# Kernel tuning notes

Hardware: AMD Instinct MI355X
Metric: run time of the kernel (lower is better)

## Reference

```python
import jax, jax.numpy as jnp
import numpy as np


def setup_inputs() -> dict:
    key = jax.random.key(0)
    kx, kw, kb = jax.random.split(key, 3)
    x = jax.random.normal(kx, (4, 2048, 4096), dtype=jnp.float32)
    weight = jax.random.normal(kw, (4096, 4096), dtype=jnp.float32) * 0.02
    bias = jax.random.normal(kb, (4096,), dtype=jnp.float32) * 0.02
    return {"x": x, "weight": weight, "bias": bias}


def _binarize_except_outliers(w):
    # Outlier mask from global weight stats (computed from w itself; in torch it
    # is cached after the first call but the values are identical every step).
    mean = jnp.mean(w)
    std = jnp.std(w, ddof=1)  # torch.std default is the unbiased estimator
    lower = mean - 1.96 * std
    upper = mean + 1.96 * std
    outliers = (w < lower) | (w > upper)
    keep = (~outliers).astype(w.dtype)
    # scaling_factor in the torch code: w[~outliers].abs().mean(-1) on the
    # flattened masked-select -> a single SCALAR, detached from the graph.
    scale = jax.lax.stop_gradient(jnp.sum(jnp.abs(w) * keep) / jnp.sum(keep))
    # NOTE: the torch code assigns STE-sign values and then immediately
    # overwrites them with w * scale, so the effective math is:
    w_bin = jnp.where(outliers, w, w * scale)
    return w_bin


def reference(x, weight, bias):
    w_bin = _binarize_except_outliers(weight)  # [out, in]
    # F.linear(x, w, b) = x @ w.T + b
    return jnp.einsum("bsi,oi->bso", x, w_bin) + bias
```

## Files before the change

kernel.cpp:

```cpp
#include <hip/hip_runtime.h>
#include <hip/hip_bf16.h>
#include <math.h>

#define MDIM 8192
#define NDIM 4096
#define KDIM 4096
#define WELEMS 16777216
#define XELEMS 33554432

typedef __attribute__((ext_vector_type(8))) short bf16x8;
typedef __attribute__((ext_vector_type(4))) float f32x4;
typedef unsigned short ushort_t;

__device__ __forceinline__ unsigned short f2bf(float f) {
  unsigned int u = __float_as_uint(f);
  u += 0x7fffu + ((u >> 16) & 1u);
  return (unsigned short)(u >> 16);
}

__device__ __forceinline__ void gload16(const void* g, void* l) {
  __builtin_amdgcn_global_load_lds(
      (const __attribute__((address_space(1))) void*)g,
      (__attribute__((address_space(3))) void*)l, 16, 0, 0);
}

template <int MODE>
__global__ __launch_bounds__(256)
void np_stage1(const float* __restrict__ w, float* __restrict__ C,
               float* __restrict__ C2, const float* __restrict__ scal) {
  __shared__ float ls[32], ls2[32];
  const int t = threadIdx.x;
  const int leaf = t >> 3, j = t & 7;
  const size_t base = (size_t)blockIdx.x * 4096 + leaf * 128 + j;
  float mean = 0.f, lower = 0.f, upper = 0.f;
  if (MODE == 1) mean = scal[0];
  if (MODE == 2) { lower = scal[1]; upper = scal[2]; }
  float r = 0.f, r2 = 0.f;
#pragma unroll
  for (int s = 0; s < 16; s++) {
    float v = w[base + s * 8];
    float tv, tv2 = 0.f;
    if (MODE == 0) tv = v;
    else if (MODE == 1) { float x = v - mean; tv = __fmul_rn(x, x); }
    else {
      bool keep = !(v < lower || v > upper);
      tv = keep ? fabsf(v) : 0.f;
      tv2 = keep ? 1.f : 0.f;
    }
    if (s == 0) { r = tv; r2 = tv2; } else { r += tv; r2 += tv2; }
  }
  r += __shfl_xor(r, 1); r += __shfl_xor(r, 2); r += __shfl_xor(r, 4);
  if (MODE == 2) { r2 += __shfl_xor(r2, 1); r2 += __shfl_xor(r2, 2); r2 += __shfl_xor(r2, 4); }
  if (j == 0) { ls[leaf] = r; if (MODE == 2) ls2[leaf] = r2; }
  __syncthreads();
  if (t == 0) {
    float tmp[32];
    for (int i = 0; i < 32; i++) tmp[i] = ls[i];
    for (int n = 32; n > 1; n >>= 1)
      for (int i = 0; i < n / 2; i++) tmp[i] = tmp[2 * i] + tmp[2 * i + 1];
    C[blockIdx.x] = tmp[0];
    if (MODE == 2) {
      for (int i = 0; i < 32; i++) tmp[i] = ls2[i];
      for (int n = 32; n > 1; n >>= 1)
        for (int i = 0; i < n / 2; i++) tmp[i] = tmp[2 * i] + tmp[2 * i + 1];
      C2[blockIdx.x] = tmp[0];
    }
  }
}

template <int MODE>
__global__ __launch_bounds__(256)
void np_stage2(const float* __restrict__ C, const float* __restrict__ C2,
               float* __restrict__ scal) {
  __shared__ float ls[256], ls2[256];
  const int t = threadIdx.x;
  {
    float v[16];
    for (int i = 0; i < 16; i++) v[i] = C[t * 16 + i];
    for (int n = 16; n > 1; n >>= 1)
      for (int i = 0; i < n / 2; i++) v[i] = v[2 * i] + v[2 * i + 1];
    ls[t] = v[0];
    if (MODE == 2) {
      for (int i = 0; i < 16; i++) v[i] = C2[t * 16 + i];
      for (int n = 16; n > 1; n >>= 1)
        for (int i = 0; i < n / 2; i++) v[i] = v[2 * i] + v[2 * i + 1];
      ls2[t] = v[0];
    }
  }
  __syncthreads();
  if (t == 0) {
    float tmp[256];
    for (int i = 0; i < 256; i++) tmp[i] = ls[i];
    for (int n = 256; n > 1; n >>= 1)
      for (int i = 0; i < n / 2; i++) tmp[i] = tmp[2 * i] + tmp[2 * i + 1];
    float S = tmp[0];
    if (MODE == 0) {
      scal[0] = S / 16777216.0f;
    } else if (MODE == 1) {
      float var = S / 16777215.0f;
      float sd = sqrtf(var);
      float mean = scal[0];
      scal[1] = mean - __fmul_rn(1.96f, sd);
      scal[2] = mean + __fmul_rn(1.96f, sd);
    } else {
      for (int i = 0; i < 256; i++) tmp[i] = ls2[i];
      for (int n = 256; n > 1; n >>= 1)
        for (int i = 0; i < n / 2; i++) tmp[i] = tmp[2 * i] + tmp[2 * i + 1];
      scal[3] = S / tmp[0];
    }
  }
}

__device__ __forceinline__ void pack8(const float* __restrict__ p, unsigned short* dst,
                                      bool dobin, float lower, float upper, float scale) {
  float4 u = *(const float4*)p;
  float4 v = *(const float4*)(p + 4);
  float f[8] = {u.x, u.y, u.z, u.w, v.x, v.y, v.z, v.w};
  unsigned int r[4];
#pragma unroll
  for (int j = 0; j < 4; j++) {
    float a = f[2 * j], b = f[2 * j + 1];
    if (dobin) {
      bool oa = (a < lower) || (a > upper);
      bool ob = (b < lower) || (b > upper);
      a = oa ? a : __fmul_rn(a, scale);
      b = ob ? b : __fmul_rn(b, scale);
    }
    r[j] = (unsigned int)f2bf(a) | ((unsigned int)f2bf(b) << 16);
  }
  *(uint4*)dst = make_uint4(r[0], r[1], r[2], r[3]);
}

__global__ __launch_bounds__(256)
void convert_w(const float* __restrict__ w, unsigned short* __restrict__ wb,
               const float* __restrict__ scal) {
  float lower = scal[1], upper = scal[2], scale = scal[3];
  int tid = blockIdx.x * blockDim.x + threadIdx.x;
  int nth = gridDim.x * blockDim.x;
  int nc = WELEMS / 8;
  for (int i = tid; i < nc; i += nth)
    pack8(w + (size_t)i * 8, wb + (size_t)i * 8, true, lower, upper, scale);
}

__global__ __launch_bounds__(256)
void convert_x(const float* __restrict__ x, unsigned short* __restrict__ xb) {
  int tid = blockIdx.x * blockDim.x + threadIdx.x;
  int nth = gridDim.x * blockDim.x;
  int nc = XELEMS / 8;
  for (int i = tid; i < nc; i += nth)
    pack8(x + (size_t)i * 8, xb + (size_t)i * 8, false, 0.f, 0.f, 0.f);
}


#define VM2  asm volatile("s_waitcnt vmcnt(2)" ::: "memory")
#define VM0  asm volatile("s_waitcnt vmcnt(0)" ::: "memory")
#define PSYNC { asm volatile("" ::: "memory"); __builtin_amdgcn_s_barrier(); asm volatile("" ::: "memory"); }

#define LDA(buf, mh) { \
  a[0][0] = *(const bf16x8*)&sA[buf][wm][((mh)*64 +  0 + fr)*64 + koo0]; \
  a[0][1] = *(const bf16x8*)&sA[buf][wm][((mh)*64 +  0 + fr)*64 + koo1]; \
  a[1][0] = *(const bf16x8*)&sA[buf][wm][((mh)*64 + 16 + fr)*64 + koo0]; \
  a[1][1] = *(const bf16x8*)&sA[buf][wm][((mh)*64 + 16 + fr)*64 + koo1]; \
  a[2][0] = *(const bf16x8*)&sA[buf][wm][((mh)*64 + 32 + fr)*64 + koo0]; \
  a[2][1] = *(const bf16x8*)&sA[buf][wm][((mh)*64 + 32 + fr)*64 + koo1]; \
  a[3][0] = *(const bf16x8*)&sA[buf][wm][((mh)*64 + 48 + fr)*64 + koo0]; \
  a[3][1] = *(const bf16x8*)&sA[buf][wm][((mh)*64 + 48 + fr)*64 + koo1]; }

#define LDB(buf, nh) { \
  b[0][0] = *(const bf16x8*)&sB[buf][wnh][(wnq*64 + (nh)*32 +  0 + fr)*64 + koo0]; \
  b[0][1] = *(const bf16x8*)&sB[buf][wnh][(wnq*64 + (nh)*32 +  0 + fr)*64 + koo1]; \
  b[1][0] = *(const bf16x8*)&sB[buf][wnh][(wnq*64 + (nh)*32 + 16 + fr)*64 + koo0]; \
  b[1][1] = *(const bf16x8*)&sB[buf][wnh][(wnq*64 + (nh)*32 + 16 + fr)*64 + koo1]; }

#define MM1(m, n, ks) acc[m][n] = __builtin_amdgcn_mfma_f32_16x16x32_bf16(a[(m)&3][ks], b[(n)&1][ks], acc[m][n], 0, 0, 0)
#define MM(mh, nh) { \
  MM1((mh)*4+0, (nh)*2+0, 0); MM1((mh)*4+0, (nh)*2+0, 1); \
  MM1((mh)*4+0, (nh)*2+1, 0); MM1((mh)*4+0, (nh)*2+1, 1); \
  MM1((mh)*4+1, (nh)*2+0, 0); MM1((mh)*4+1, (nh)*2+0, 1); \
  MM1((mh)*4+1, (nh)*2+1, 0); MM1((mh)*4+1, (nh)*2+1, 1); \
  MM1((mh)*4+2, (nh)*2+0, 0); MM1((mh)*4+2, (nh)*2+0, 1); \
  MM1((mh)*4+2, (nh)*2+1, 0); MM1((mh)*4+2, (nh)*2+1, 1); \
  MM1((mh)*4+3, (nh)*2+0, 0); MM1((mh)*4+3, (nh)*2+0, 1); \
  MM1((mh)*4+3, (nh)*2+1, 0); MM1((mh)*4+3, (nh)*2+1, 1); }

#define STGA(buf, q, ku) { \
  gload16(xbp + aoff[0][q] + (ku), &sA[buf][0][(q)*4096 + t8]); \
  gload16(xbp + aoff[1][q] + (ku), &sA[buf][1][(q)*4096 + t8]); }
#define STGB(buf, h, ku) { \
  gload16(wbp + boff[h][0] + (ku), &sB[buf][h][t8]); \
  gload16(wbp + boff[h][1] + (ku), &sB[buf][h][4096 + t8]); }

__global__ __launch_bounds__(512, 2)
void gemm256(const unsigned short* __restrict__ xbp, const unsigned short* __restrict__ wbp,
             const float* __restrict__ bias, float* __restrict__ out) {
  __shared__ unsigned short sA[2][2][8192];
  __shared__ unsigned short sB[2][2][8192];

  const int bid = blockIdx.x;
  const int swz = (bid & 7) * 64 + (bid >> 3);
  const int bm = swz >> 4;
  const int bn = swz & 15;

  const int t = threadIdx.x;
  const int lane = t & 63;
  const int wid = t >> 6;
  const int wm = wid >> 2;
  const int wn = wid & 3;
  const int wnh = wn >> 1;
  const int wnq = wn & 1;
  const int fr = lane & 15;
  const int ko = (lane >> 4) * 8;
  const int xr = (fr & 7) << 3;
  const int koo0 = ko ^ xr;
  const int koo1 = (32 + ko) ^ xr;

  const int t8 = t * 8;
  const int rl = t >> 3;
  const int cs = ((t & 7) * 8) ^ ((rl & 7) << 3);
  size_t aoff[2][2], boff[2][2];
#pragma unroll
  for (int h = 0; h < 2; h++)
#pragma unroll
    for (int q = 0; q < 2; q++) {
      aoff[h][q] = (size_t)(bm * 256 + h * 128 + q * 64 + rl) * KDIM + cs;
      boff[h][q] = (size_t)(bn * 256 + h * 128 + q * 64 + rl) * KDIM + cs;
    }

  f32x4 acc[8][4];
#pragma unroll
  for (int i = 0; i < 8; i++)
#pragma unroll
    for (int j = 0; j < 4; j++) acc[i][j] = {0.f, 0.f, 0.f, 0.f};

  bf16x8 a[4][2], b[2][2];

  STGA(0, 0, 0); STGA(0, 1, 0); STGB(0, 0, 0); STGB(0, 1, 0);
  STGA(1, 0, 64);

  const int NIT = KDIM / 128;
  for (int it = 0; it < NIT; ++it) {
    const bool last = (it == NIT - 1);
    const int kuA = it * 128;
    const int kuB = kuA + 64;
    const int kuN = kuA + 128;

    VM2; PSYNC;
    LDA(0, 0); LDB(0, 0);
    STGA(1, 1, kuB);
    __builtin_amdgcn_s_setprio(1); MM(0, 0); __builtin_amdgcn_s_setprio(0);

    PSYNC;
    LDB(0, 1);
    STGB(1, 0, kuB);
    __builtin_amdgcn_s_setprio(1); MM(0, 1); __builtin_amdgcn_s_setprio(0);

    PSYNC;
    LDA(0, 1);
    STGB(1, 1, kuB);
    __builtin_amdgcn_s_setprio(1); MM(1, 1); __builtin_amdgcn_s_setprio(0);

    PSYNC;
    LDB(0, 0);
    if (!last) STGA(0, 0, kuN);
    __builtin_amdgcn_s_setprio(1); MM(1, 0); __builtin_amdgcn_s_setprio(0);

    if (last) { VM0; } else { VM2; }
    PSYNC;
    LDA(1, 0); LDB(1, 0);
    if (!last) STGA(0, 1, kuN);
    __builtin_amdgcn_s_setprio(1); MM(0, 0); __builtin_amdgcn_s_setprio(0);

    PSYNC;
    LDB(1, 1);
    if (!last) STGB(0, 0, kuN);
    __builtin_amdgcn_s_setprio(1); MM(0, 1); __builtin_amdgcn_s_setprio(0);

    PSYNC;
    LDA(1, 1);
    if (!last) STGB(0, 1, kuN);
    __builtin_amdgcn_s_setprio(1); MM(1, 1); __builtin_amdgcn_s_setprio(0);

    PSYNC;
    LDB(1, 0);
    if (!last) STGA(1, 0, kuA + 192);
    __builtin_amdgcn_s_setprio(1); MM(1, 0); __builtin_amdgcn_s_setprio(0);
  }

#pragma unroll
  for (int nn = 0; nn < 4; ++nn) {
    const int col = bn * 256 + wn * 64 + nn * 16 + (lane & 15);
    const float bv = bias[col];
#pragma unroll
    for (int m = 0; m < 8; ++m) {
      const int row0 = bm * 256 + wm * 128 + m * 16 + (lane >> 4) * 4;
#pragma unroll
      for (int q = 0; q < 4; ++q)
        out[(size_t)(row0 + q) * NDIM + col] = acc[m][nn][q] + bv;
    }
  }
}

template <bool A_BF16, bool B_BF16>
__global__ __launch_bounds__(256)
void gemm_bt(const void* __restrict__ Av, const void* __restrict__ Bv,
             const float* __restrict__ bias, float* __restrict__ out,
             const float* __restrict__ scal) {
  __shared__ unsigned short sAt[2][128 * 32];
  __shared__ unsigned short sBt[2][128 * 32];
  float lower = 0.f, upper = 0.f, scale = 0.f;
  if constexpr (!B_BF16) { lower = scal[1]; upper = scal[2]; scale = scal[3]; }
  const unsigned short* Ab = (const unsigned short*)Av;
  const float* Af = (const float*)Av;
  const unsigned short* Bb = (const unsigned short*)Bv;
  const float* Bf = (const float*)Bv;
  int bid = blockIdx.x;
  int swz = (bid & 7) * 256 + (bid >> 3);
  int bm = swz >> 5, bn = swz & 31;
  const int t = threadIdx.x, lane = t & 63, wid = t >> 6;
  const int wm = wid >> 1, wn = wid & 1;
  const int e0 = t * 8, e1 = e0 + 2048;
  const size_t aOff0 = (size_t)(bm * 128 + (e0 >> 5)) * KDIM + (e0 & 31);
  const size_t aOff1 = (size_t)(bm * 128 + (e1 >> 5)) * KDIM + (e1 & 31);
  const size_t bOff0 = (size_t)(bn * 128 + (e0 >> 5)) * KDIM + (e0 & 31);
  const size_t bOff1 = (size_t)(bn * 128 + (e1 >> 5)) * KDIM + (e1 & 31);
  f32x4 acc[4][4];
#pragma unroll
  for (int i = 0; i < 4; i++)
#pragma unroll
    for (int j = 0; j < 4; j++) acc[i][j] = {0.f, 0.f, 0.f, 0.f};
  auto stage = [&](int buf, int k0) {
    if constexpr (A_BF16) {
      gload16(Ab + aOff0 + k0, &sAt[buf][e0]);
      gload16(Ab + aOff1 + k0, &sAt[buf][e1]);
    } else {
      pack8(Af + aOff0 + k0, &sAt[buf][e0], false, 0.f, 0.f, 0.f);
      pack8(Af + aOff1 + k0, &sAt[buf][e1], false, 0.f, 0.f, 0.f);
    }
    if constexpr (B_BF16) {
      gload16(Bb + bOff0 + k0, &sBt[buf][e0]);
      gload16(Bb + bOff1 + k0, &sBt[buf][e1]);
    } else {
      pack8(Bf + bOff0 + k0, &sBt[buf][e0], true, lower, upper, scale);
      pack8(Bf + bOff1 + k0, &sBt[buf][e1], true, lower, upper, scale);
    }
  };
  stage(0, 0);
  const int NT = KDIM / 32;
  const int ko = (lane >> 4) * 8, fr = lane & 15;
  for (int tt = 0; tt < NT; ++tt) {
    int cur = tt & 1;
    __syncthreads();
    if (tt + 1 < NT) stage(cur ^ 1, (tt + 1) * 32);
    bf16x8 a[4], b[4];
#pragma unroll
    for (int i = 0; i < 4; i++) {
      a[i] = *(const bf16x8*)&sAt[cur][(wm * 64 + i * 16 + fr) * 32 + ko];
      b[i] = *(const bf16x8*)&sBt[cur][(wn * 64 + i * 16 + fr) * 32 + ko];
    }
#pragma unroll
    for (int i = 0; i < 4; i++)
#pragma unroll
      for (int j = 0; j < 4; j++)
        acc[i][j] = __builtin_amdgcn_mfma_f32_16x16x32_bf16(a[i], b[j], acc[i][j], 0, 0, 0);
  }
  const int colbase = bn * 128 + wn * 64 + (lane & 15);
  const int rowbase = bm * 128 + wm * 64 + (lane >> 4) * 4;
#pragma unroll
  for (int j = 0; j < 4; j++) {
    int col = colbase + j * 16;
    float bv = bias[col];
#pragma unroll
    for (int i = 0; i < 4; i++) {
      int row0 = rowbase + i * 16;
#pragma unroll
      for (int q = 0; q < 4; q++)
        out[(size_t)(row0 + q) * NDIM + col] = acc[i][j][q] + bv;
    }
  }
}

extern "C" void kernel_launch(void* const* d_in, const int* in_sizes, int n_in,
                              void* d_out, int out_size, void* d_ws, size_t ws_size,
                              hipStream_t stream) {
  const float* x = (const float*)d_in[0];
  const float* w = (const float*)d_in[1];
  const float* bias = (const float*)d_in[2];
  float* out = (float*)d_out;
  char* ws = (char*)d_ws;

  const size_t xb_b = (size_t)XELEMS * 2;
  const size_t wb_b = (size_t)WELEMS * 2;
  const size_t c_b = 4 * 4096 * sizeof(float);
  const bool full = ws_size >= xb_b + wb_b + c_b + 64;
  const bool wonly = !full && ws_size >= wb_b + c_b + 64;

  unsigned short *xb = nullptr, *wb = nullptr;
  float *C1, *scal;
  if (full) {
    xb = (unsigned short*)ws;
    wb = (unsigned short*)(ws + xb_b);
    C1 = (float*)(ws + xb_b + wb_b);
  } else if (wonly) {
    wb = (unsigned short*)ws;
    C1 = (float*)(ws + wb_b);
  } else {
    C1 = (float*)ws;
  }
  float* C2 = C1 + 4096;
  float* C3 = C2 + 4096;
  float* C4 = C3 + 4096;
  scal = C4 + 4096;

  np_stage1<0><<<dim3(4096), dim3(256), 0, stream>>>(w, C1, nullptr, scal);
  np_stage2<0><<<dim3(1), dim3(256), 0, stream>>>(C1, nullptr, scal);
  np_stage1<1><<<dim3(4096), dim3(256), 0, stream>>>(w, C2, nullptr, scal);
  np_stage2<1><<<dim3(1), dim3(256), 0, stream>>>(C2, nullptr, scal);
  np_stage1<2><<<dim3(4096), dim3(256), 0, stream>>>(w, C3, C4, scal);
  np_stage2<2><<<dim3(1), dim3(256), 0, stream>>>(C3, C4, scal);

  if (full) {
    convert_w<<<dim3(2048), dim3(256), 0, stream>>>(w, wb, scal);
    convert_x<<<dim3(4096), dim3(256), 0, stream>>>(x, xb);
    gemm256<<<dim3(512), dim3(512), 0, stream>>>(xb, wb, bias, out);
  } else if (wonly) {
    convert_w<<<dim3(2048), dim3(256), 0, stream>>>(w, wb, scal);
    gemm_bt<false, true><<<dim3(2048), dim3(256), 0, stream>>>(x, wb, bias, out, scal);
  } else {
    gemm_bt<false, false><<<dim3(2048), dim3(256), 0, stream>>>(x, w, bias, out, scal);
  }
}
```

Before: 423.9 us.

## Restructure GEMM main loop into barrier-bracketed load and MFMA phases

```diff
diff --git a/kernel.cpp b/kernel.cpp
--- a/kernel.cpp
+++ b/kernel.cpp
@@ -10,7 +10,6 @@
 
 typedef __attribute__((ext_vector_type(8))) short bf16x8;
 typedef __attribute__((ext_vector_type(4))) float f32x4;
-typedef unsigned short ushort_t;
 
 __device__ __forceinline__ unsigned short f2bf(float f) {
   unsigned int u = __float_as_uint(f);
@@ -154,6 +153,7 @@
 
 #define VM2  asm volatile("s_waitcnt vmcnt(2)" ::: "memory")
 #define VM0  asm volatile("s_waitcnt vmcnt(0)" ::: "memory")
+#define LGK8 asm volatile("s_waitcnt lgkmcnt(8)" ::: "memory")
 #define PSYNC { asm volatile("" ::: "memory"); __builtin_amdgcn_s_barrier(); asm volatile("" ::: "memory"); }
 
 #define LDA(buf, mh) { \
@@ -173,15 +173,15 @@
   b[1][1] = *(const bf16x8*)&sB[buf][wnh][(wnq*64 + (nh)*32 + 16 + fr)*64 + koo1]; }
 
 #define MM1(m, n, ks) acc[m][n] = __builtin_amdgcn_mfma_f32_16x16x32_bf16(a[(m)&3][ks], b[(n)&1][ks], acc[m][n], 0, 0, 0)
+#define MMKS(mh, nh, ks) { \
+  MM1((mh)*4+0, (nh)*2+0, ks); MM1((mh)*4+0, (nh)*2+1, ks); \
+  MM1((mh)*4+1, (nh)*2+0, ks); MM1((mh)*4+1, (nh)*2+1, ks); \
+  MM1((mh)*4+2, (nh)*2+0, ks); MM1((mh)*4+2, (nh)*2+1, ks); \
+  MM1((mh)*4+3, (nh)*2+0, ks); MM1((mh)*4+3, (nh)*2+1, ks); }
 #define MM(mh, nh) { \
-  MM1((mh)*4+0, (nh)*2+0, 0); MM1((mh)*4+0, (nh)*2+0, 1); \
-  MM1((mh)*4+0, (nh)*2+1, 0); MM1((mh)*4+0, (nh)*2+1, 1); \
-  MM1((mh)*4+1, (nh)*2+0, 0); MM1((mh)*4+1, (nh)*2+0, 1); \
-  MM1((mh)*4+1, (nh)*2+1, 0); MM1((mh)*4+1, (nh)*2+1, 1); \
-  MM1((mh)*4+2, (nh)*2+0, 0); MM1((mh)*4+2, (nh)*2+0, 1); \
-  MM1((mh)*4+2, (nh)*2+1, 0); MM1((mh)*4+2, (nh)*2+1, 1); \
-  MM1((mh)*4+3, (nh)*2+0, 0); MM1((mh)*4+3, (nh)*2+0, 1); \
-  MM1((mh)*4+3, (nh)*2+1, 0); MM1((mh)*4+3, (nh)*2+1, 1); }
+  __builtin_amdgcn_s_setprio(1); \
+  MMKS(mh, nh, 0); MMKS(mh, nh, 1); \
+  __builtin_amdgcn_s_setprio(0); }
 
 #define STGA(buf, q, ku) { \
   gload16(xbp + aoff[0][q] + (ku), &sA[buf][0][(q)*4096 + t8]); \
@@ -236,54 +236,57 @@
 
   STGA(0, 0, 0); STGA(0, 1, 0); STGB(0, 0, 0); STGB(0, 1, 0);
   STGA(1, 0, 64);
+  VM2; PSYNC;
 
   const int NIT = KDIM / 128;
   for (int it = 0; it < NIT; ++it) {
     const bool last = (it == NIT - 1);
-    const int kuA = it * 128;
-    const int kuB = kuA + 64;
-    const int kuN = kuA + 128;
-
-    VM2; PSYNC;
+    const int kuB = it * 128 + 64;
+    const int kuN = kuB + 64;
+
     LDA(0, 0); LDB(0, 0);
     STGA(1, 1, kuB);
-    __builtin_amdgcn_s_setprio(1); MM(0, 0); __builtin_amdgcn_s_setprio(0);
-
-    PSYNC;
+    LGK8; PSYNC;
+    MM(0, 0); PSYNC;
+
     LDB(0, 1);
     STGB(1, 0, kuB);
-    __builtin_amdgcn_s_setprio(1); MM(0, 1); __builtin_amdgcn_s_setprio(0);
-
-    PSYNC;
+    PSYNC;
+    MM(0, 1); PSYNC;
+
     LDA(0, 1);
     STGB(1, 1, kuB);
-    __builtin_amdgcn_s_setprio(1); MM(1, 1); __builtin_amdgcn_s_setprio(0);
-
-    PSYNC;
+    PSYNC;
+    MM(1, 1); PSYNC;
+
     LDB(0, 0);
     if (!last) STGA(0, 0, kuN);
-    __builtin_amdgcn_s_setprio(1); MM(1, 0); __builtin_amdgcn_s_setprio(0);
-
     if (last) { VM0; } else { VM2; }
     PSYNC;
+    MM(1, 0); PSYNC;
+
     LDA(1, 0); LDB(1, 0);
     if (!last) STGA(0, 1, kuN);
-    __builtin_amdgcn_s_setprio(1); MM(0, 0); __builtin_amdgcn_s_setprio(0);
-
-    PSYNC;
+    LGK8; PSYNC;
+    MM(0, 0); PSYNC;
+
     LDB(1, 1);
     if (!last) STGB(0, 0, kuN);
-    __builtin_amdgcn_s_setprio(1); MM(0, 1); __builtin_amdgcn_s_setprio(0);
-
-    PSYNC;
+    PSYNC;
+    MM(0, 1); PSYNC;
+
     LDA(1, 1);
     if (!last) STGB(0, 1, kuN);
-    __builtin_amdgcn_s_setprio(1); MM(1, 1); __builtin_amdgcn_s_setprio(0);
-
-    PSYNC;
+    PSYNC;
+    MM(1, 1); PSYNC;
+
     LDB(1, 0);
-    if (!last) STGA(1, 0, kuA + 192);
-    __builtin_amdgcn_s_setprio(1); MM(1, 0); __builtin_amdgcn_s_setprio(0);
+    if (!last) {
+      STGA(1, 0, kuN + 64);
+      VM2;
+    }
+    PSYNC;
+    MM(1, 0); PSYNC;
   }
 
 #pragma unroll
```

Measured after the change: 431.5 us. Within noise of the previous version (+1.8%).
